# Optimization experiments

Measured on AMD Instinct MI355X. Metric: run time of the kernel, lower is better.

Reference implementation:

```python
import jax, jax.numpy as jnp
import numpy as np

TOKENS, HIDDEN, FFN = 4096, 4096, 14336
SCALE = 0.02  # keep activations in a sane range


def setup_inputs() -> dict:
    key = jax.random.key(0)
    k1, k2, k3, k4 = jax.random.split(key, 4)
    x = jax.random.normal(k1, (TOKENS, HIDDEN), dtype=jnp.float32)
    expert_w1 = jax.random.normal(k2, (FFN, HIDDEN), dtype=jnp.float32) * SCALE
    expert_v1 = jax.random.normal(k3, (FFN, HIDDEN), dtype=jnp.float32) * SCALE
    expert_w2 = jax.random.normal(k4, (FFN, HIDDEN), dtype=jnp.float32) * SCALE
    return {"x": x, "expert_w1": expert_w1, "expert_v1": expert_v1, "expert_w2": expert_w2}


def reference(x, expert_w1, expert_v1, expert_w2):
    # gate/up projections: [T, H] @ [H, F] -> [T, F]
    gate = jnp.einsum('th,fh->tf', x, expert_w1)
    up = jnp.einsum('th,fh->tf', x, expert_v1)
    inter = jax.nn.silu(gate) * up            # fused SwiGLU intermediate [T, F]
    down = jnp.einsum('tf,fh->th', inter, expert_w2)  # [T, H]
    return down
```

## Files before the change

kernel.cpp:

```cpp
#include <hip/hip_runtime.h>
#include <hip/hip_bf16.h>
#include <stdint.h>

#define TOKENS 4096
#define HIDDEN 4096
#define FFN    14336

typedef __attribute__((ext_vector_type(8))) short bf16x8;
typedef __attribute__((ext_vector_type(4))) float f32x4;
typedef __attribute__((ext_vector_type(8))) unsigned short u16x8;

typedef __attribute__((address_space(3))) void lds_void_t;
typedef const __attribute__((address_space(1))) void gbl_void_t;

static __device__ __forceinline__ unsigned short f2b(float f) {
  union { float f; unsigned int u; } v; v.f = f;
  unsigned int u = v.u;
  return (unsigned short)((u + 0x7FFFu + ((u >> 16) & 1u)) >> 16);
}

__global__ void cvt_kernel(const float* __restrict__ in, unsigned short* __restrict__ out, long n) {
  long idx = (long)blockIdx.x * blockDim.x + threadIdx.x;
  long stride = (long)gridDim.x * blockDim.x;
  for (long i = idx * 4; i < n; i += stride * 4) {
    const float4 v = *reinterpret_cast<const float4*>(in + i);
    ushort4 o;
    o.x = f2b(v.x); o.y = f2b(v.y); o.z = f2b(v.z); o.w = f2b(v.w);
    *reinterpret_cast<ushort4*>(out + i) = o;
  }
}

__global__ void transpose_cvt_kernel(const float* __restrict__ in, unsigned short* __restrict__ out) {
  __shared__ float tile[64][65];
  const int f0 = blockIdx.x * 64;
  const int h0 = blockIdx.y * 64;
  const int t = threadIdx.x;
  const int rcol = (t & 15) * 4;
  const int rrow = t >> 4;
#pragma unroll
  for (int it = 0; it < 4; ++it) {
    int r = rrow + it * 16;
    const float4 v = *reinterpret_cast<const float4*>(in + (long)(f0 + r) * HIDDEN + h0 + rcol);
    tile[r][rcol] = v.x; tile[r][rcol + 1] = v.y; tile[r][rcol + 2] = v.z; tile[r][rcol + 3] = v.w;
  }
  __syncthreads();
  const int wrow = t >> 2;
  const int wc = (t & 3) * 16;
  u16x8 lo, hi;
#pragma unroll
  for (int j = 0; j < 8; ++j) lo[j] = f2b(tile[wc + j][wrow]);
#pragma unroll
  for (int j = 0; j < 8; ++j) hi[j] = f2b(tile[wc + 8 + j][wrow]);
  u16x8* dst = reinterpret_cast<u16x8*>(out + (long)(h0 + wrow) * FFN + f0 + wc);
  dst[0] = lo; dst[1] = hi;
}

#define MFMA16(a, b, c) __builtin_amdgcn_mfma_f32_16x16x32_bf16((a), (b), (c), 0, 0, 0)
#define SBAR()  __builtin_amdgcn_s_barrier()

static __device__ __forceinline__ int xcd_chunk(int bid, int nwg) {
  return (bid & 7) * (nwg >> 3) + (bid >> 3);
}

__global__ __launch_bounds__(512, 2)
void gateup256p_kernel(const unsigned short* __restrict__ X,
                       const unsigned short* __restrict__ W1,
                       const unsigned short* __restrict__ V1,
                       unsigned short* __restrict__ Inter,
                       int j0, int j1) {
  __shared__ unsigned short sh[81920];
  const int tid = threadIdx.x, lane = tid & 63, wid = tid >> 6;
  const int wm = wid >> 2, wn = wid & 3;
  const int p = blockIdx.x;
  const int bm = p & 15;
  const int bnl = p >> 4;
  const int sr = tid >> 3;
  const int scb = (((tid & 7) ^ (sr & 7)) << 4);
  const int l15 = lane & 15;
  const int cb0 = (((lane >> 4) * 16) ^ ((lane & 7) << 4));
  const int cb1 = ((64 + (lane >> 4) * 16) ^ ((lane & 7) << 4));

  const unsigned short* Ap = X + (long)(bm * 256) * HIDDEN;

  auto LDA8 = [&](bf16x8* a, int bufA, int cb) {
    const char* base = (const char*)sh + bufA * 32768 + wm * 16384 + l15 * 128 + cb;
#pragma unroll
    for (int m = 0; m < 8; ++m) a[m] = *(const bf16x8*)(base + m * 2048);
  };
  auto LDW2 = [&](bf16x8* w, int b3, int cb) {
    const char* base = (const char*)sh + 65536 + b3 * 32768 + (wn * 32 + l15) * 128 + cb;
    w[0] = *(const bf16x8*)(base);
    w[1] = *(const bf16x8*)(base + 2048);
  };
  auto LDV2 = [&](bf16x8* v, int b3, int cb) {
    const char* base = (const char*)sh + 65536 + b3 * 32768 + 16384 + (wn * 32 + l15) * 128 + cb;
    v[0] = *(const bf16x8*)(base);
    v[1] = *(const bf16x8*)(base + 2048);
  };

  for (int j = j0; j < j1; ++j) {
    const int bn = j * 16 + bnl;
    const unsigned short* Wp = W1 + (long)(bn * 128) * HIDDEN;
    const unsigned short* Vp = V1 + (long)(bn * 128) * HIDDEN;

    auto STA = [&](int u, int bufA, int t) {
      const unsigned short* src = Ap + (long)(u * 64 + sr) * HIDDEN + t * 64 + (scb >> 1);
      unsigned short* dst = sh + bufA * 16384 + u * 4096 + tid * 8;
      __builtin_amdgcn_global_load_lds((gbl_void_t*)src, (lds_void_t*)dst, 16, 0, 0);
    };
    auto STW = [&](int u, int b3, int t) {
      const unsigned short* src = Wp + (long)(u * 64 + sr) * HIDDEN + t * 64 + (scb >> 1);
      unsigned short* dst = sh + 32768 + b3 * 16384 + u * 4096 + tid * 8;
      __builtin_amdgcn_global_load_lds((gbl_void_t*)src, (lds_void_t*)dst, 16, 0, 0);
    };
    auto STV = [&](int u, int b3, int t) {
      const unsigned short* src = Vp + (long)(u * 64 + sr) * HIDDEN + t * 64 + (scb >> 1);
      unsigned short* dst = sh + 32768 + b3 * 16384 + 8192 + u * 4096 + tid * 8;
      __builtin_amdgcn_global_load_lds((gbl_void_t*)src, (lds_void_t*)dst, 16, 0, 0);
    };

    f32x4 accg[8][2] = {};
    f32x4 accu[8][2] = {};

    STW(0, 0, 0); STW(1, 0, 0); STV(0, 0, 0); STV(1, 0, 0);
    STA(0, 0, 0); STA(1, 0, 0); STA(2, 0, 0); STA(3, 0, 0);
    STW(0, 1, 1); STW(1, 1, 1); STV(0, 1, 1); STV(1, 1, 1);

    bf16x8 a[8], w[2], v[2];
    const int NT = HIDDEN / 64;
    for (int t = 0; t < NT; ++t) {
      const int curA = t & 1, nxtA = curA ^ 1;
      const int b3 = t % 3, b3w = (t + 2) % 3;
      asm volatile("s_waitcnt lgkmcnt(0)" ::: "memory");
      if (t + 1 < NT) { asm volatile("s_waitcnt vmcnt(4)" ::: "memory"); }
      else            { asm volatile("s_waitcnt vmcnt(0)" ::: "memory"); }
      SBAR();
      if (t + 1 < NT) { STA(0, nxtA, t + 1); STA(1, nxtA, t + 1);
                        STA(2, nxtA, t + 1); STA(3, nxtA, t + 1); }
      if (t + 2 < NT) { STW(0, b3w, t + 2); STW(1, b3w, t + 2);
                        STV(0, b3w, t + 2); STV(1, b3w, t + 2); }
      LDA8(a, curA, cb0); LDW2(w, b3, cb0); LDV2(v, b3, cb0);
      __builtin_amdgcn_s_setprio(1);
#pragma unroll
      for (int m = 0; m < 8; ++m) {
        accg[m][0] = MFMA16(a[m], w[0], accg[m][0]);
        accg[m][1] = MFMA16(a[m], w[1], accg[m][1]);
      }
#pragma unroll
      for (int m = 0; m < 8; ++m) {
        accu[m][0] = MFMA16(a[m], v[0], accu[m][0]);
        accu[m][1] = MFMA16(a[m], v[1], accu[m][1]);
      }
      __builtin_amdgcn_s_setprio(0);
      LDA8(a, curA, cb1); LDW2(w, b3, cb1); LDV2(v, b3, cb1);
      __builtin_amdgcn_s_setprio(1);
#pragma unroll
      for (int m = 0; m < 8; ++m) {
        accg[m][0] = MFMA16(a[m], w[0], accg[m][0]);
        accg[m][1] = MFMA16(a[m], w[1], accg[m][1]);
      }
#pragma unroll
      for (int m = 0; m < 8; ++m) {
        accu[m][0] = MFMA16(a[m], v[0], accu[m][0]);
        accu[m][1] = MFMA16(a[m], v[1], accu[m][1]);
      }
      __builtin_amdgcn_s_setprio(0);
    }
    const int r0 = (lane >> 4) * 4;
#pragma unroll
    for (int m = 0; m < 8; ++m)
#pragma unroll
      for (int n = 0; n < 2; ++n)
#pragma unroll
        for (int r = 0; r < 4; ++r) {
          const float g = accg[m][n][r];
          const float u = accu[m][n][r];
          const float s = g / (1.0f + __expf(-g));
          const int row = bm * 256 + wm * 128 + m * 16 + r0 + r;
          const int col = bn * 128 + wn * 32 + n * 16 + l15;
          Inter[(long)row * FFN + col] = f2b(s * u);
        }
    asm volatile("s_waitcnt vmcnt(0)" ::: "memory");
  }
}

__global__ __launch_bounds__(512, 2)
void down256_kernel(const unsigned short* __restrict__ Inter,
                    const unsigned short* __restrict__ W2t,
                    float* __restrict__ Out) {
  __shared__ unsigned short sh[81920];
  const int tid = threadIdx.x, lane = tid & 63, wid = tid >> 6;
  const int wm = wid >> 2, wn = wid & 3;
  const int swz = xcd_chunk(blockIdx.x, (TOKENS / 256) * (HIDDEN / 256));
  const int bm = swz & 15;
  const int bn = swz >> 4;
  const int sr = tid >> 3;
  const int scb = (((tid & 7) ^ (sr & 7)) << 4);
  const int l15 = lane & 15;
  const int cb0 = (((lane >> 4) * 16) ^ ((lane & 7) << 4));
  const int cb1 = ((64 + (lane >> 4) * 16) ^ ((lane & 7) << 4));

  const unsigned short* Ap = Inter + (long)(bm * 256) * FFN;
  const unsigned short* Bp = W2t + (long)(bn * 256) * FFN;

  f32x4 acc[8][4] = {};

  auto STA = [&](int h, int bufA, int t) {
    const unsigned short* src = Ap + (long)(h * 128 + sr) * FFN + t * 64 + (scb >> 1);
    unsigned short* dst = sh + bufA * 16384 + h * 8192 + tid * 8;
    __builtin_amdgcn_global_load_lds((gbl_void_t*)src, (lds_void_t*)dst, 16, 0, 0);
    __builtin_amdgcn_global_load_lds((gbl_void_t*)(src + 64L * FFN), (lds_void_t*)(dst + 4096), 16, 0, 0);
  };
  auto STB = [&](int h, int s3, int t) {
    const unsigned short* src = Bp + (long)(h * 128 + sr) * FFN + t * 64 + (scb >> 1);
    unsigned short* dst = sh + 32768 + s3 * 16384 + h * 8192 + tid * 8;
    __builtin_amdgcn_global_load_lds((gbl_void_t*)src, (lds_void_t*)dst, 16, 0, 0);
    __builtin_amdgcn_global_load_lds((gbl_void_t*)(src + 64L * FFN), (lds_void_t*)(dst + 4096), 16, 0, 0);
  };
  auto LDA8 = [&](bf16x8* a, int bufA, int cb) {
    const char* base = (const char*)sh + bufA * 32768 + wm * 16384 + l15 * 128 + cb;
#pragma unroll
    for (int m = 0; m < 8; ++m) a[m] = *(const bf16x8*)(base + m * 2048);
  };
  auto LDB2 = [&](bf16x8* b, int s3, int cb, int np) {
    const char* base = (const char*)sh + 65536 + s3 * 32768 + (wn >> 1) * 16384 +
                       ((wn & 1) * 64 + l15) * 128 + cb;
    b[2 * np]     = *(const bf16x8*)(base + (2 * np) * 2048);
    b[2 * np + 1] = *(const bf16x8*)(base + (2 * np + 1) * 2048);
  };

  STB(0, 0, 0); STB(1, 0, 0);
  STA(0, 0, 0); STA(1, 0, 0);
  STB(0, 1, 1); STB(1, 1, 1);

  bf16x8 a[8], b[4];
  const int NT = FFN / 64;
  for (int t = 0; t < NT; ++t) {
    const int curA = t & 1, nxtA = curA ^ 1;
    const int b3 = t % 3, b3w = (t + 2) % 3;
    asm volatile("s_waitcnt lgkmcnt(0)" ::: "memory");
    if (t + 1 < NT) { asm volatile("s_waitcnt vmcnt(4)" ::: "memory"); }
    else            { asm volatile("s_waitcnt vmcnt(0)" ::: "memory"); }
    SBAR();
    if (t + 1 < NT) { STA(0, nxtA, t + 1); STA(1, nxtA, t + 1); }
    if (t + 2 < NT) { STB(0, b3w, t + 2); STB(1, b3w, t + 2); }
    LDA8(a, curA, cb0); LDB2(b, b3, cb0, 0); LDB2(b, b3, cb0, 1);
    __builtin_amdgcn_s_setprio(1);
#pragma unroll
    for (int m = 0; m < 8; ++m) {
      acc[m][0] = MFMA16(a[m], b[0], acc[m][0]);
      acc[m][1] = MFMA16(a[m], b[1], acc[m][1]);
    }
#pragma unroll
    for (int m = 0; m < 8; ++m) {
      acc[m][2] = MFMA16(a[m], b[2], acc[m][2]);
      acc[m][3] = MFMA16(a[m], b[3], acc[m][3]);
    }
    __builtin_amdgcn_s_setprio(0);
    LDA8(a, curA, cb1); LDB2(b, b3, cb1, 0); LDB2(b, b3, cb1, 1);
    __builtin_amdgcn_s_setprio(1);
#pragma unroll
    for (int m = 0; m < 8; ++m) {
      acc[m][0] = MFMA16(a[m], b[0], acc[m][0]);
      acc[m][1] = MFMA16(a[m], b[1], acc[m][1]);
    }
#pragma unroll
    for (int m = 0; m < 8; ++m) {
      acc[m][2] = MFMA16(a[m], b[2], acc[m][2]);
      acc[m][3] = MFMA16(a[m], b[3], acc[m][3]);
    }
    __builtin_amdgcn_s_setprio(0);
  }
  const int r0 = (lane >> 4) * 4;
#pragma unroll
  for (int m = 0; m < 8; ++m)
#pragma unroll
    for (int n = 0; n < 4; ++n)
#pragma unroll
      for (int r = 0; r < 4; ++r) {
        const int row = bm * 256 + wm * 128 + m * 16 + r0 + r;
        const int col = bn * 256 + wn * 64 + n * 16 + l15;
        Out[(long)row * HIDDEN + col] = acc[m][n][r];
      }
}

__device__ __forceinline__ void stage_tile_128(const unsigned short* __restrict__ g, long ldk,
                                               unsigned short* lds, int wave, int lane) {
#pragma unroll
  for (int it = 0; it < 2; ++it) {
    const int row = (it * 4 + wave) * 16 + (lane >> 2);
    const int kcol = (lane & 3) * 8;
    const unsigned short* src = g + (long)row * ldk + kcol;
    unsigned short* dst = lds + row * 32 + kcol;
    __builtin_amdgcn_global_load_lds((gbl_void_t*)src, (lds_void_t*)dst, 16, 0, 0);
  }
}

__global__ __launch_bounds__(256, 2)
void down_nt_kernel(const unsigned short* __restrict__ Inter,
                    const float* __restrict__ W2,
                    float* __restrict__ Out) {
  __shared__ unsigned short As[128 * 32];
  __shared__ unsigned short Bs[128 * 32];
  const int t = threadIdx.x;
  const int lane = t & 63;
  const int wave = t >> 6;
  const int bm = blockIdx.x & 31;
  const int bn = blockIdx.x >> 5;
  const int wm = (wave >> 1) * 64;
  const int wn = (wave & 1) * 64;
  const unsigned short* gA = Inter + (long)(bm * 128) * FFN;

  f32x4 acc[4][4] = {};
  const int fr = lane & 15;
  const int kg = (lane >> 4) * 8;
  const int p = lane & 15;
  const int h0 = wave * 32 + (lane >> 4) * 8;
  const float* gB = W2 + bn * 128 + h0;

  for (int kt = 0; kt < FFN; kt += 32) {
    __syncthreads();
    stage_tile_128(gA + kt, FFN, As, wave, lane);
    const float* r0p = gB + (long)(kt + 2 * p) * HIDDEN;
    const float* r1p = r0p + HIDDEN;
    const float4 a0 = *reinterpret_cast<const float4*>(r0p);
    const float4 a1 = *reinterpret_cast<const float4*>(r0p + 4);
    const float4 b0 = *reinterpret_cast<const float4*>(r1p);
    const float4 b1 = *reinterpret_cast<const float4*>(r1p + 4);
    unsigned short lo[8], hi[8];
    lo[0] = f2b(a0.x); lo[1] = f2b(a0.y); lo[2] = f2b(a0.z); lo[3] = f2b(a0.w);
    lo[4] = f2b(a1.x); lo[5] = f2b(a1.y); lo[6] = f2b(a1.z); lo[7] = f2b(a1.w);
    hi[0] = f2b(b0.x); hi[1] = f2b(b0.y); hi[2] = f2b(b0.z); hi[3] = f2b(b0.w);
    hi[4] = f2b(b1.x); hi[5] = f2b(b1.y); hi[6] = f2b(b1.z); hi[7] = f2b(b1.w);
#pragma unroll
    for (int j = 0; j < 8; ++j) {
      const unsigned int pack = (unsigned int)lo[j] | ((unsigned int)hi[j] << 16);
      *reinterpret_cast<unsigned int*>(&Bs[(h0 + j) * 32 + 2 * p]) = pack;
    }
    __syncthreads();
    bf16x8 a[4], b[4];
#pragma unroll
    for (int m = 0; m < 4; ++m)
      a[m] = *reinterpret_cast<const bf16x8*>(&As[(wm + m * 16 + fr) * 32 + kg]);
#pragma unroll
    for (int n = 0; n < 4; ++n)
      b[n] = *reinterpret_cast<const bf16x8*>(&Bs[(wn + n * 16 + fr) * 32 + kg]);
#pragma unroll
    for (int m = 0; m < 4; ++m)
#pragma unroll
      for (int n = 0; n < 4; ++n)
        acc[m][n] = MFMA16(a[m], b[n], acc[m][n]);
  }
  const int r0 = (lane >> 4) * 4;
#pragma unroll
  for (int m = 0; m < 4; ++m)
#pragma unroll
    for (int n = 0; n < 4; ++n)
#pragma unroll
      for (int r = 0; r < 4; ++r) {
        const int row = bm * 128 + wm + m * 16 + r0 + r;
        const int col = bn * 128 + wn + n * 16 + fr;
        Out[(long)row * HIDDEN + col] = acc[m][n][r];
      }
}

extern "C" void kernel_launch(void* const* d_in, const int* in_sizes, int n_in,
                              void* d_out, int out_size, void* d_ws, size_t ws_size,
                              hipStream_t stream) {
  const float* x  = (const float*)d_in[0];
  const float* w1 = (const float*)d_in[1];
  const float* v1 = (const float*)d_in[2];
  const float* w2 = (const float*)d_in[3];
  float* out = (float*)d_out;

  const size_t REQ_SMALL = 385875968UL;
  const size_t REQ_FULL  = 503316480UL;
  if (ws_size < REQ_SMALL) return;
  const bool full = (ws_size >= REQ_FULL);
  char* ws = (char*)d_ws;
  unsigned short* xb     = (unsigned short*)(ws);
  unsigned short* w1b    = (unsigned short*)(ws + 33554432L);
  unsigned short* v1b    = (unsigned short*)(ws + 150994944L);
  unsigned short* interb = (unsigned short*)(ws + 268435456L);
  unsigned short* w2tb   = (unsigned short*)(ws + 385875968L);

  const long HALF1 = 8192L * HIDDEN;
  const long HALF2 = (long)(FFN - 8192) * HIDDEN;

  hipLaunchKernelGGL(cvt_kernel, dim3(2048), dim3(256), 0, stream, x, xb, (long)TOKENS * HIDDEN);
  hipLaunchKernelGGL(cvt_kernel, dim3(2048), dim3(256), 0, stream, w1, w1b, HALF1);
  hipLaunchKernelGGL(cvt_kernel, dim3(2048), dim3(256), 0, stream, v1, v1b, HALF1);
  hipLaunchKernelGGL(gateup256p_kernel, dim3(256), dim3(512), 0, stream,
                     xb, w1b, v1b, interb, 0, 4);
  hipLaunchKernelGGL(cvt_kernel, dim3(2048), dim3(256), 0, stream, w1 + HALF1, w1b + HALF1, HALF2);
  hipLaunchKernelGGL(cvt_kernel, dim3(2048), dim3(256), 0, stream, v1 + HALF1, v1b + HALF1, HALF2);
  hipLaunchKernelGGL(gateup256p_kernel, dim3(256), dim3(512), 0, stream,
                     xb, w1b, v1b, interb, 4, 7);

  if (full) {
    hipLaunchKernelGGL(transpose_cvt_kernel, dim3(FFN / 64, HIDDEN / 64), dim3(256), 0, stream, w2, w2tb);
    hipLaunchKernelGGL(down256_kernel, dim3((TOKENS / 256) * (HIDDEN / 256)), dim3(512), 0, stream,
                       interb, w2tb, out);
  } else {
    hipLaunchKernelGGL(down_nt_kernel, dim3((TOKENS / 128) * (HIDDEN / 128)), dim3(256), 0, stream,
                       interb, w2, out);
  }
}
```

Before: 1.369 ms.

## Shrink GEMM tiles to raise occupancy and drop persistent gate/up loop

Both the gate/up and down GEMMs move from large 256x256 (or 256x128 dual) tiles with a 64-wide K step and about 160KB of LDS to smaller tiles with a 32-wide K step and about 56KB of LDS, with launch bounds raised to four blocks per CU. The gate/up kernel is no longer persistent over a j-range; it launches one workgroup per 256x64 output tile and uses an XCD-aware block swizzle. This is meant to hide latency through more resident waves and a larger grid. In exchange, operand reuse per byte loaded drops, K iterations double, and the XOR LDS swizzle is removed, which may bring back bank conflicts.

```diff
diff --git a/kernel.cpp b/kernel.cpp
--- a/kernel.cpp
+++ b/kernel.cpp
@@ -62,224 +62,185 @@
   return (bid & 7) * (nwg >> 3) + (bid >> 3);
 }
 
-__global__ __launch_bounds__(512, 2)
-void gateup256p_kernel(const unsigned short* __restrict__ X,
+__global__ __launch_bounds__(512, 4)
+void gateup256c_kernel(const unsigned short* __restrict__ X,
                        const unsigned short* __restrict__ W1,
                        const unsigned short* __restrict__ V1,
                        unsigned short* __restrict__ Inter,
-                       int j0, int j1) {
-  __shared__ unsigned short sh[81920];
+                       int bnBase, int nwg) {
+  __shared__ unsigned short sh[28672];
   const int tid = threadIdx.x, lane = tid & 63, wid = tid >> 6;
-  const int wm = wid >> 2, wn = wid & 3;
-  const int p = blockIdx.x;
-  const int bm = p & 15;
-  const int bnl = p >> 4;
-  const int sr = tid >> 3;
-  const int scb = (((tid & 7) ^ (sr & 7)) << 4);
+  const int wm = wid >> 1, wn = wid & 1;
+  const int swz = xcd_chunk(blockIdx.x, nwg);
+  const int bm = swz & 15;
+  const int bn = bnBase + (swz >> 4);
   const int l15 = lane & 15;
-  const int cb0 = (((lane >> 4) * 16) ^ ((lane & 7) << 4));
-  const int cb1 = ((64 + (lane >> 4) * 16) ^ ((lane & 7) << 4));
-
-  const unsigned short* Ap = X + (long)(bm * 256) * HIDDEN;
-
-  auto LDA8 = [&](bf16x8* a, int bufA, int cb) {
-    const char* base = (const char*)sh + bufA * 32768 + wm * 16384 + l15 * 128 + cb;
-#pragma unroll
-    for (int m = 0; m < 8; ++m) a[m] = *(const bf16x8*)(base + m * 2048);
-  };
-  auto LDW2 = [&](bf16x8* w, int b3, int cb) {
-    const char* base = (const char*)sh + 65536 + b3 * 32768 + (wn * 32 + l15) * 128 + cb;
+  const int kb = (lane >> 4) * 16;
+
+  const unsigned short* Ap = X  + (long)(bm * 256) * HIDDEN;
+  const unsigned short* Wp = W1 + (long)(bn * 64) * HIDDEN;
+  const unsigned short* Vp = V1 + (long)(bn * 64) * HIDDEN;
+
+  f32x4 accg[4][2] = {};
+  f32x4 accu[4][2] = {};
+
+  auto STA = [&](int bufA, int t) {
+    const unsigned short* src = Ap + (long)(tid >> 2) * HIDDEN + t * 32 + (tid & 3) * 8;
+    unsigned short* dst = sh + bufA * 8192 + tid * 8;
+    __builtin_amdgcn_global_load_lds((gbl_void_t*)src, (lds_void_t*)dst, 16, 0, 0);
+    __builtin_amdgcn_global_load_lds((gbl_void_t*)(src + 128L * HIDDEN), (lds_void_t*)(dst + 4096), 16, 0, 0);
+  };
+  auto STWV = [&](int s3, int t) {
+    if (tid < 256) {
+      const unsigned short* src = Wp + (long)(tid >> 2) * HIDDEN + t * 32 + (tid & 3) * 8;
+      unsigned short* dst = sh + 16384 + s3 * 4096 + tid * 8;
+      __builtin_amdgcn_global_load_lds((gbl_void_t*)src, (lds_void_t*)dst, 16, 0, 0);
+    } else {
+      const int t2 = tid - 256;
+      const unsigned short* src = Vp + (long)(t2 >> 2) * HIDDEN + t * 32 + (t2 & 3) * 8;
+      unsigned short* dst = sh + 16384 + s3 * 4096 + 2048 + t2 * 8;
+      __builtin_amdgcn_global_load_lds((gbl_void_t*)src, (lds_void_t*)dst, 16, 0, 0);
+    }
+  };
+  auto LDA4 = [&](bf16x8* a, int bufA) {
+    const char* base = (const char*)sh + bufA * 16384 + (wm * 64 + l15) * 64 + kb;
+#pragma unroll
+    for (int m = 0; m < 4; ++m) a[m] = *(const bf16x8*)(base + m * 1024);
+  };
+  auto LDW2 = [&](bf16x8* w, int s3) {
+    const char* base = (const char*)sh + 32768 + s3 * 8192 + (wn * 32 + l15) * 64 + kb;
     w[0] = *(const bf16x8*)(base);
-    w[1] = *(const bf16x8*)(base + 2048);
-  };
-  auto LDV2 = [&](bf16x8* v, int b3, int cb) {
-    const char* base = (const char*)sh + 65536 + b3 * 32768 + 16384 + (wn * 32 + l15) * 128 + cb;
+    w[1] = *(const bf16x8*)(base + 1024);
+  };
+  auto LDV2 = [&](bf16x8* v, int s3) {
+    const char* base = (const char*)sh + 32768 + s3 * 8192 + 4096 + (wn * 32 + l15) * 64 + kb;
     v[0] = *(const bf16x8*)(base);
-    v[1] = *(const bf16x8*)(base + 2048);
-  };
-
-  for (int j = j0; j < j1; ++j) {
-    const int bn = j * 16 + bnl;
-    const unsigned short* Wp = W1 + (long)(bn * 128) * HIDDEN;
-    const unsigned short* Vp = V1 + (long)(bn * 128) * HIDDEN;
-
-    auto STA = [&](int u, int bufA, int t) {
-      const unsigned short* src = Ap + (long)(u * 64 + sr) * HIDDEN + t * 64 + (scb >> 1);
-      unsigned short* dst = sh + bufA * 16384 + u * 4096 + tid * 8;
-      __builtin_amdgcn_global_load_lds((gbl_void_t*)src, (lds_void_t*)dst, 16, 0, 0);
-    };
-    auto STW = [&](int u, int b3, int t) {
-      const unsigned short* src = Wp + (long)(u * 64 + sr) * HIDDEN + t * 64 + (scb >> 1);
-      unsigned short* dst = sh + 32768 + b3 * 16384 + u * 4096 + tid * 8;
-      __builtin_amdgcn_global_load_lds((gbl_void_t*)src, (lds_void_t*)dst, 16, 0, 0);
-    };
-    auto STV = [&](int u, int b3, int t) {
-      const unsigned short* src = Vp + (long)(u * 64 + sr) * HIDDEN + t * 64 + (scb >> 1);
-      unsigned short* dst = sh + 32768 + b3 * 16384 + 8192 + u * 4096 + tid * 8;
-      __builtin_amdgcn_global_load_lds((gbl_void_t*)src, (lds_void_t*)dst, 16, 0, 0);
-    };
-
-    f32x4 accg[8][2] = {};
-    f32x4 accu[8][2] = {};
-
-    STW(0, 0, 0); STW(1, 0, 0); STV(0, 0, 0); STV(1, 0, 0);
-    STA(0, 0, 0); STA(1, 0, 0); STA(2, 0, 0); STA(3, 0, 0);
-    STW(0, 1, 1); STW(1, 1, 1); STV(0, 1, 1); STV(1, 1, 1);
-
-    bf16x8 a[8], w[2], v[2];
-    const int NT = HIDDEN / 64;
-    for (int t = 0; t < NT; ++t) {
-      const int curA = t & 1, nxtA = curA ^ 1;
-      const int b3 = t % 3, b3w = (t + 2) % 3;
-      asm volatile("s_waitcnt lgkmcnt(0)" ::: "memory");
-      if (t + 1 < NT) { asm volatile("s_waitcnt vmcnt(4)" ::: "memory"); }
-      else            { asm volatile("s_waitcnt vmcnt(0)" ::: "memory"); }
-      SBAR();
-      if (t + 1 < NT) { STA(0, nxtA, t + 1); STA(1, nxtA, t + 1);
-                        STA(2, nxtA, t + 1); STA(3, nxtA, t + 1); }
-      if (t + 2 < NT) { STW(0, b3w, t + 2); STW(1, b3w, t + 2);
-                        STV(0, b3w, t + 2); STV(1, b3w, t + 2); }
-      LDA8(a, curA, cb0); LDW2(w, b3, cb0); LDV2(v, b3, cb0);
-      __builtin_amdgcn_s_setprio(1);
-#pragma unroll
-      for (int m = 0; m < 8; ++m) {
-        accg[m][0] = MFMA16(a[m], w[0], accg[m][0]);
-        accg[m][1] = MFMA16(a[m], w[1], accg[m][1]);
+    v[1] = *(const bf16x8*)(base + 1024);
+  };
+
+  STWV(0, 0);
+  STA(0, 0);
+  STWV(1, 1);
+
+  bf16x8 a[4], w[2], v[2];
+  const int NT = HIDDEN / 32;
+  for (int t = 0; t < NT; ++t) {
+    const int curA = t & 1, nxtA = curA ^ 1;
+    const int s3 = t % 3, s3w = (t + 2) % 3;
+    asm volatile("s_waitcnt lgkmcnt(0)" ::: "memory");
+    if (t + 1 < NT) { asm volatile("s_waitcnt vmcnt(1)" ::: "memory"); }
+    else            { asm volatile("s_waitcnt vmcnt(0)" ::: "memory"); }
+    SBAR();
+    if (t + 1 < NT) STA(nxtA, t + 1);
+    if (t + 2 < NT) STWV(s3w, t + 2);
+    LDA4(a, curA); LDW2(w, s3); LDV2(v, s3);
+    __builtin_amdgcn_s_setprio(1);
+#pragma unroll
+    for (int m = 0; m < 4; ++m) {
+      accg[m][0] = MFMA16(a[m], w[0], accg[m][0]);
+      accg[m][1] = MFMA16(a[m], w[1], accg[m][1]);
+    }
+#pragma unroll
+    for (int m = 0; m < 4; ++m) {
+      accu[m][0] = MFMA16(a[m], v[0], accu[m][0]);
+      accu[m][1] = MFMA16(a[m], v[1], accu[m][1]);
+    }
+    __builtin_amdgcn_s_setprio(0);
+  }
+  const int r0 = (lane >> 4) * 4;
+#pragma unroll
+  for (int m = 0; m < 4; ++m)
+#pragma unroll
+    for (int n = 0; n < 2; ++n)
+#pragma unroll
+      for (int r = 0; r < 4; ++r) {
+        const float g = accg[m][n][r];
+        const float u = accu[m][n][r];
+        const float s = g / (1.0f + __expf(-g));
+        const int row = bm * 256 + wm * 64 + m * 16 + r0 + r;
+        const int col = bn * 64 + wn * 32 + n * 16 + l15;
+        Inter[(long)row * FFN + col] = f2b(s * u);
       }
-#pragma unroll
-      for (int m = 0; m < 8; ++m) {
-        accu[m][0] = MFMA16(a[m], v[0], accu[m][0]);
-        accu[m][1] = MFMA16(a[m], v[1], accu[m][1]);
-      }
-      __builtin_amdgcn_s_setprio(0);
-      LDA8(a, curA, cb1); LDW2(w, b3, cb1); LDV2(v, b3, cb1);
-      __builtin_amdgcn_s_setprio(1);
-#pragma unroll
-      for (int m = 0; m < 8; ++m) {
-        accg[m][0] = MFMA16(a[m], w[0], accg[m][0]);
-        accg[m][1] = MFMA16(a[m], w[1], accg[m][1]);
-      }
-#pragma unroll
-      for (int m = 0; m < 8; ++m) {
-        accu[m][0] = MFMA16(a[m], v[0], accu[m][0]);
-        accu[m][1] = MFMA16(a[m], v[1], accu[m][1]);
-      }
-      __builtin_amdgcn_s_setprio(0);
-    }
-    const int r0 = (lane >> 4) * 4;
-#pragma unroll
-    for (int m = 0; m < 8; ++m)
-#pragma unroll
-      for (int n = 0; n < 2; ++n)
-#pragma unroll
-        for (int r = 0; r < 4; ++r) {
-          const float g = accg[m][n][r];
-          const float u = accu[m][n][r];
-          const float s = g / (1.0f + __expf(-g));
-          const int row = bm * 256 + wm * 128 + m * 16 + r0 + r;
-          const int col = bn * 128 + wn * 32 + n * 16 + l15;
-          Inter[(long)row * FFN + col] = f2b(s * u);
-        }
-    asm volatile("s_waitcnt vmcnt(0)" ::: "memory");
-  }
-}
-
-__global__ __launch_bounds__(512, 2)
-void down256_kernel(const unsigned short* __restrict__ Inter,
-                    const unsigned short* __restrict__ W2t,
-                    float* __restrict__ Out) {
-  __shared__ unsigned short sh[81920];
+}
+
+__global__ __launch_bounds__(512, 4)
+void down256c_kernel(const unsigned short* __restrict__ Inter,
+                     const unsigned short* __restrict__ W2t,
+                     float* __restrict__ Out) {
+  __shared__ unsigned short sh[28672];
   const int tid = threadIdx.x, lane = tid & 63, wid = tid >> 6;
-  const int wm = wid >> 2, wn = wid & 3;
-  const int swz = xcd_chunk(blockIdx.x, (TOKENS / 256) * (HIDDEN / 256));
+  const int wm = wid >> 1, wn = wid & 1;
+  const int swz = xcd_chunk(blockIdx.x, (TOKENS / 256) * (HIDDEN / 128));
   const int bm = swz & 15;
   const int bn = swz >> 4;
-  const int sr = tid >> 3;
-  const int scb = (((tid & 7) ^ (sr & 7)) << 4);
   const int l15 = lane & 15;
-  const int cb0 = (((lane >> 4) * 16) ^ ((lane & 7) << 4));
-  const int cb1 = ((64 + (lane >> 4) * 16) ^ ((lane & 7) << 4));
+  const int kb = (lane >> 4) * 16;
 
   const unsigned short* Ap = Inter + (long)(bm * 256) * FFN;
-  const unsigned short* Bp = W2t + (long)(bn * 256) * FFN;
-
-  f32x4 acc[8][4] = {};
-
-  auto STA = [&](int h, int bufA, int t) {
-    const unsigned short* src = Ap + (long)(h * 128 + sr) * FFN + t * 64 + (scb >> 1);
-    unsigned short* dst = sh + bufA * 16384 + h * 8192 + tid * 8;
+  const unsigned short* Bp = W2t + (long)(bn * 128) * FFN;
+
+  f32x4 acc[4][4] = {};
+
+  auto STA = [&](int bufA, int t) {
+    const unsigned short* src = Ap + (long)(tid >> 2) * FFN + t * 32 + (tid & 3) * 8;
+    unsigned short* dst = sh + bufA * 8192 + tid * 8;
     __builtin_amdgcn_global_load_lds((gbl_void_t*)src, (lds_void_t*)dst, 16, 0, 0);
-    __builtin_amdgcn_global_load_lds((gbl_void_t*)(src + 64L * FFN), (lds_void_t*)(dst + 4096), 16, 0, 0);
-  };
-  auto STB = [&](int h, int s3, int t) {
-    const unsigned short* src = Bp + (long)(h * 128 + sr) * FFN + t * 64 + (scb >> 1);
-    unsigned short* dst = sh + 32768 + s3 * 16384 + h * 8192 + tid * 8;
+    __builtin_amdgcn_global_load_lds((gbl_void_t*)(src + 128L * FFN), (lds_void_t*)(dst + 4096), 16, 0, 0);
+  };
+  auto STB = [&](int s3, int t) {
+    const unsigned short* src = Bp + (long)(tid >> 2) * FFN + t * 32 + (tid & 3) * 8;
+    unsigned short* dst = sh + 16384 + s3 * 4096 + tid * 8;
     __builtin_amdgcn_global_load_lds((gbl_void_t*)src, (lds_void_t*)dst, 16, 0, 0);
-    __builtin_amdgcn_global_load_lds((gbl_void_t*)(src + 64L * FFN), (lds_void_t*)(dst + 4096), 16, 0, 0);
-  };
-  auto LDA8 = [&](bf16x8* a, int bufA, int cb) {
-    const char* base = (const char*)sh + bufA * 32768 + wm * 16384 + l15 * 128 + cb;
-#pragma unroll
-    for (int m = 0; m < 8; ++m) a[m] = *(const bf16x8*)(base + m * 2048);
-  };
-  auto LDB2 = [&](bf16x8* b, int s3, int cb, int np) {
-    const char* base = (const char*)sh + 65536 + s3 * 32768 + (wn >> 1) * 16384 +
-                       ((wn & 1) * 64 + l15) * 128 + cb;
-    b[2 * np]     = *(const bf16x8*)(base + (2 * np) * 2048);
-    b[2 * np + 1] = *(const bf16x8*)(base + (2 * np + 1) * 2048);
-  };
-
-  STB(0, 0, 0); STB(1, 0, 0);
-  STA(0, 0, 0); STA(1, 0, 0);
-  STB(0, 1, 1); STB(1, 1, 1);
-
-  bf16x8 a[8], b[4];
-  const int NT = FFN / 64;
+  };
+  auto LDA4 = [&](bf16x8* a, int bufA) {
+    const char* base = (const char*)sh + bufA * 16384 + (wm * 64 + l15) * 64 + kb;
+#pragma unroll
+    for (int m = 0; m < 4; ++m) a[m] = *(const bf16x8*)(base + m * 1024);
+  };
+  auto LDB4 = [&](bf16x8* b, int s3) {
+    const char* base = (const char*)sh + 32768 + s3 * 8192 + (wn * 64 + l15) * 64 + kb;
+#pragma unroll
+    for (int n = 0; n < 4; ++n) b[n] = *(const bf16x8*)(base + n * 1024);
+  };
+
+  STB(0, 0);
+  STA(0, 0);
+  STB(1, 1);
+
+  bf16x8 a[4], b[4];
+  const int NT = FFN / 32;
   for (int t = 0; t < NT; ++t) {
     const int curA = t & 1, nxtA = curA ^ 1;
-    const int b3 = t % 3, b3w = (t + 2) % 3;
+    const int s3 = t % 3, s3w = (t + 2) % 3;
     asm volatile("s_waitcnt lgkmcnt(0)" ::: "memory");
-    if (t + 1 < NT) { asm volatile("s_waitcnt vmcnt(4)" ::: "memory"); }
+    if (t + 1 < NT) { asm volatile("s_waitcnt vmcnt(1)" ::: "memory"); }
     else            { asm volatile("s_waitcnt vmcnt(0)" ::: "memory"); }
     SBAR();
-    if (t + 1 < NT) { STA(0, nxtA, t + 1); STA(1, nxtA, t + 1); }
-    if (t + 2 < NT) { STB(0, b3w, t + 2); STB(1, b3w, t + 2); }
-    LDA8(a, curA, cb0); LDB2(b, b3, cb0, 0); LDB2(b, b3, cb0, 1);
+    if (t + 1 < NT) STA(nxtA, t + 1);
+    if (t + 2 < NT) STB(s3w, t + 2);
+    LDA4(a, curA); LDB4(b, s3);
     __builtin_amdgcn_s_setprio(1);
 #pragma unroll
-    for (int m = 0; m < 8; ++m) {
+    for (int m = 0; m < 4; ++m) {
       acc[m][0] = MFMA16(a[m], b[0], acc[m][0]);
       acc[m][1] = MFMA16(a[m], b[1], acc[m][1]);
     }
 #pragma unroll
-    for (int m = 0; m < 8; ++m) {
+    for (int m = 0; m < 4; ++m) {
       acc[m][2] = MFMA16(a[m], b[2], acc[m][2]);
       acc[m][3] = MFMA16(a[m], b[3], acc[m][3]);
     }
     __builtin_amdgcn_s_setprio(0);
-    LDA8(a, curA, cb1); LDB2(b, b3, cb1, 0); LDB2(b, b3, cb1, 1);
-    __builtin_amdgcn_s_setprio(1);
-#pragma unroll
-    for (int m = 0; m < 8; ++m) {
-      acc[m][0] = MFMA16(a[m], b[0], acc[m][0]);
-      acc[m][1] = MFMA16(a[m], b[1], acc[m][1]);
-    }
-#pragma unroll
-    for (int m = 0; m < 8; ++m) {
-      acc[m][2] = MFMA16(a[m], b[2], acc[m][2]);
-      acc[m][3] = MFMA16(a[m], b[3], acc[m][3]);
-    }
-    __builtin_amdgcn_s_setprio(0);
   }
   const int r0 = (lane >> 4) * 4;
 #pragma unroll
-  for (int m = 0; m < 8; ++m)
+  for (int m = 0; m < 4; ++m)
 #pragma unroll
     for (int n = 0; n < 4; ++n)
 #pragma unroll
       for (int r = 0; r < 4; ++r) {
-        const int row = bm * 256 + wm * 128 + m * 16 + r0 + r;
-        const int col = bn * 256 + wn * 64 + n * 16 + l15;
+        const int row = bm * 256 + wm * 64 + m * 16 + r0 + r;
+        const int col = bn * 128 + wn * 64 + n * 16 + l15;
         Out[(long)row * HIDDEN + col] = acc[m][n][r];
       }
 }
@@ -390,16 +351,16 @@
   hipLaunchKernelGGL(cvt_kernel, dim3(2048), dim3(256), 0, stream, x, xb, (long)TOKENS * HIDDEN);
   hipLaunchKernelGGL(cvt_kernel, dim3(2048), dim3(256), 0, stream, w1, w1b, HALF1);
   hipLaunchKernelGGL(cvt_kernel, dim3(2048), dim3(256), 0, stream, v1, v1b, HALF1);
-  hipLaunchKernelGGL(gateup256p_kernel, dim3(256), dim3(512), 0, stream,
-                     xb, w1b, v1b, interb, 0, 4);
+  hipLaunchKernelGGL(gateup256c_kernel, dim3(16 * 128), dim3(512), 0, stream,
+                     xb, w1b, v1b, interb, 0, 16 * 128);
   hipLaunchKernelGGL(cvt_kernel, dim3(2048), dim3(256), 0, stream, w1 + HALF1, w1b + HALF1, HALF2);
   hipLaunchKernelGGL(cvt_kernel, dim3(2048), dim3(256), 0, stream, v1 + HALF1, v1b + HALF1, HALF2);
-  hipLaunchKernelGGL(gateup256p_kernel, dim3(256), dim3(512), 0, stream,
-                     xb, w1b, v1b, interb, 4, 7);
+  hipLaunchKernelGGL(gateup256c_kernel, dim3(16 * 96), dim3(512), 0, stream,
+                     xb, w1b, v1b, interb, 128, 16 * 96);
 
   if (full) {
     hipLaunchKernelGGL(transpose_cvt_kernel, dim3(FFN / 64, HIDDEN / 64), dim3(256), 0, stream, w2, w2tb);
-    hipLaunchKernelGGL(down256_kernel, dim3((TOKENS / 256) * (HIDDEN / 256)), dim3(512), 0, stream,
+    hipLaunchKernelGGL(down256c_kernel, dim3((TOKENS / 256) * (HIDDEN / 128)), dim3(512), 0, stream,
                        interb, w2tb, out);
   } else {
     hipLaunchKernelGGL(down_nt_kernel, dim3((TOKENS / 128) * (HIDDEN / 128)), dim3(256), 0, stream,
```

Measured after the change: 1.633 ms. 19.3% more time.
